# Performance work log

Measured on AMD Instinct MI355X. Metric: run time of the kernel, lower is better.

## Reference

```python
import jax, jax.numpy as jnp
import numpy as np

B = 1048576
H = 256


def _parity_W():
    # W[i,j,k] = 1 if (i+j+k+1) % 2 == 0  <=>  (i+j+k) odd
    idx = jnp.arange(2)
    s = idx[:, None, None] + idx[None, :, None] + idx[None, None, :]
    return (s % 2 == 1).astype(jnp.float32)


def setup_inputs() -> dict:
    key = jax.random.key(0)
    ks = jax.random.split(key, 7)
    x = jax.random.normal(ks[0], (B, 3), dtype=jnp.float32)
    w1 = jax.random.normal(ks[1], (H, 3), dtype=jnp.float32) * (1.0 / np.sqrt(3))
    b1 = jax.random.normal(ks[2], (H,), dtype=jnp.float32) * 0.01
    w2 = jax.random.normal(ks[3], (H, H), dtype=jnp.float32) * (1.0 / np.sqrt(H))
    b2 = jax.random.normal(ks[4], (H,), dtype=jnp.float32) * 0.01
    w3 = jax.random.normal(ks[5], (3, H), dtype=jnp.float32) * (1.0 / np.sqrt(H))
    b3 = jax.random.normal(ks[6], (3,), dtype=jnp.float32) * 0.01
    return {"x": x, "w1": w1, "b1": b1, "w2": w2, "b2": b2, "w3": w3, "b3": b3}


def reference(x, w1, b1, w2, b2, w3, b3):
    # MLP: 3 -> H -> H -> 3 with ReLU
    h = jax.nn.relu(x @ w1.T + b1)          # (B, H)
    h = jax.nn.relu(h @ w2.T + b2)          # (B, H)
    logitC = h @ w3.T + b3                  # (B, 3)

    eps = 1e-05
    sig = jax.nn.sigmoid(logitC)            # (B, 3)
    p_pos = (sig + eps) / (1.0 + 2.0 * eps)
    p_neg = (1.0 - sig + eps) / (1.0 + 2.0 * eps)
    p = jnp.stack([p_neg, p_pos], axis=-1)  # (B, 3, 2): per-concept Bernoulli probs

    W = _parity_W()                          # (2, 2, 2) XOR-parity indicator
    pred1 = jnp.einsum('bi,bj,bk,ijk->b', p[:, 0], p[:, 1], p[:, 2], W)  # (B,)
    pred = jnp.stack([1.0 - pred1, pred1], axis=1)  # (B, 2)
    pred = (pred + 0.001) / (1.0 + 2.0 * 0.001)
    return pred, logitC
```

## Files before the change

### kernel.cpp

```cpp
#include <hip/hip_runtime.h>

typedef _Float16 f16;
typedef _Float16 f16x8 __attribute__((ext_vector_type(8)));
typedef float f32x16 __attribute__((ext_vector_type(16)));
typedef unsigned int u32;
typedef unsigned int u32x4 __attribute__((ext_vector_type(4)));

#define THREADS 512
#define MTILE   128
#define NBLK    256

#define H1_OFF   0
#define XS_OFF   131072
#define PART_OFF 134144
#define LDS_BYTES 158720

template <int I0>
static __device__ __forceinline__ u32x4 relu_pack8(const f32x16& h) {
  const float c0 = fmaxf(h[I0+0], 0.f), c1 = fmaxf(h[I0+1], 0.f);
  const float c2 = fmaxf(h[I0+2], 0.f), c3 = fmaxf(h[I0+3], 0.f);
  const float c4 = fmaxf(h[I0+4], 0.f), c5 = fmaxf(h[I0+5], 0.f);
  const float c6 = fmaxf(h[I0+6], 0.f), c7 = fmaxf(h[I0+7], 0.f);
  u32 P = __builtin_bit_cast(u32, __builtin_amdgcn_cvt_pkrtz(c0, c1));
  u32 Q = __builtin_bit_cast(u32, __builtin_amdgcn_cvt_pkrtz(c2, c3));
  u32 R = __builtin_bit_cast(u32, __builtin_amdgcn_cvt_pkrtz(c4, c5));
  u32 S = __builtin_bit_cast(u32, __builtin_amdgcn_cvt_pkrtz(c6, c7));
  asm("v_permlane32_swap_b32 %0, %1" : "+v"(P), "+v"(R));
  asm("v_permlane32_swap_b32 %0, %1" : "+v"(Q), "+v"(S));
  u32x4 w; w[0] = P; w[1] = Q; w[2] = R; w[3] = S;
  return w;
}

__global__ __launch_bounds__(THREADS, 1)
void fused_mlp_parity(const float* __restrict__ x,
                      const float* __restrict__ w1,
                      const float* __restrict__ b1,
                      const float* __restrict__ w2,
                      const float* __restrict__ b2,
                      const float* __restrict__ w3,
                      const float* __restrict__ b3,
                      float* __restrict__ out, int Bsz) {
  __shared__ __align__(128) unsigned char lds[LDS_BYTES];
  const int tid  = threadIdx.x;
  const int lane = tid & 63;
  const int wave = tid >> 6;
  const int arow = lane & 31;
  const int half = lane >> 5;
  const int grp  = wave >> 2;

  const int ntiles = Bsz / MTILE;
  const int tpb    = ntiles / NBLK;
  const int t0     = blockIdx.x * tpb;

  float* xsf   = (float*)(lds + XS_OFF);
  float* partf = (float*)(lds + PART_OFF);

  {
    const float4* xg = (const float4*)x;
    if (tid < 96)                      ((float4*)xsf)[tid]            = xg[(size_t)t0*96 + tid];
    else if (tid >= 128 && tid < 224)  ((float4*)xsf)[96 + tid - 128] = xg[(size_t)(t0+1)*96 + (tid-128)];
  }

  const int col = (wave << 5) + arow;
  f16x8 w2A[16];
#pragma unroll
  for (int ks = 0; ks < 16; ++ks) {
    const float* src = w2 + (size_t)col*256 + ks*16 + half*8;
    float4 u0 = *(const float4*)src;
    float4 u1 = *(const float4*)(src + 4);
    f16x8 v;
    v[0]=(f16)u0.x; v[1]=(f16)u0.y; v[2]=(f16)u0.z; v[3]=(f16)u0.w;
    v[4]=(f16)u1.x; v[5]=(f16)u1.y; v[6]=(f16)u1.z; v[7]=(f16)u1.w;
    w2A[ks] = v;
  }
  f16x8 w1A = {};
  if (half == 0) {
    w1A[0] = (f16)w1[col*3+0]; w1A[1] = (f16)w1[col*3+1];
    w1A[2] = (f16)w1[col*3+2]; w1A[3] = (f16)b1[col];
  }
  f16x8 b2A = {};  if (half == 0) b2A[0] = (f16)b2[col];
  f16x8 ones = {}; if (half == 0) ones[0] = (f16)1.0f;
  f16x8 w3A[2];
#pragma unroll
  for (int q = 0; q < 2; ++q) {
    f16x8 v = {};
    if (arow < 3) {
#pragma unroll
      for (int j = 0; j < 8; ++j)
        v[j] = (f16)w3[arow*256 + (wave<<5) + q*16 + half*8 + j];
    }
    w3A[q] = v;
  }
  const float b3r0 = b3[0], b3r1 = b3[1], b3r2 = b3[2];
  const size_t outL = (size_t)Bsz * 2;
  const u32 rk = ((u32)(arow & 15)) << 4;
  const u32 cb = (u32)half << 4;

  auto PHASE_B = [&](int buf) {
    unsigned char* h1b = lds + H1_OFF + (u32)buf*65536;
    const float* xb_src = xsf + (u32)buf*384;
#pragma unroll
    for (int nt = 0; nt < 4; ++nt) {
      const int r = nt*32 + arow;
      f16x8 xb = {};
      if (half == 0) {
        const float* xr = xb_src + r*3;
        xb[0] = (f16)xr[0]; xb[1] = (f16)xr[1]; xb[2] = (f16)xr[2];
        xb[3] = (f16)1.0f;
      }
      f32x16 h = {};
      h = __builtin_amdgcn_mfma_f32_32x32x16_f16(w1A, xb, h, 0,0,0);
      const u32 rowbase = ((u32)r << 9);
      {
        u32x4 w = relu_pack8<0>(h);
        const u32 slot = (u32)(((wave<<5) + 0)*2 + half*16);
        *(u32x4*)(h1b + rowbase + (slot ^ rk)) = w;
      }
      {
        u32x4 w = relu_pack8<8>(h);
        const u32 slot = (u32)(((wave<<5) + 16)*2 + half*16);
        *(u32x4*)(h1b + rowbase + (slot ^ rk)) = w;
      }
    }
  };

  auto PHASE_CE = [&](int buf) {
    const unsigned char* h1b = lds + H1_OFF + (u32)buf*65536;
#pragma unroll
    for (int ntp = 0; ntp < 2; ++ntp) {
      f32x16 acc0, acc1;
      {
        f32x16 z = {};
        acc0 = __builtin_amdgcn_mfma_f32_32x32x16_f16(b2A, ones, z, 0,0,0);
        acc1 = __builtin_amdgcn_mfma_f32_32x32x16_f16(b2A, ones, z, 0,0,0);
      }
      const u32 row0 = (u32)((ntp*2 + 0)*32 + arow) << 9;
      const u32 row1 = (u32)((ntp*2 + 1)*32 + arow) << 9;
#pragma unroll
      for (int ks = 0; ks < 16; ++ks) {
        const u32 coff = ((((u32)ks) << 5) + cb) ^ rk;
        f16x8 fr0 = *(const f16x8*)(h1b + row0 + coff);
        f16x8 fr1 = *(const f16x8*)(h1b + row1 + coff);
        acc0 = __builtin_amdgcn_mfma_f32_32x32x16_f16(w2A[ks], fr0, acc0, 0,0,0);
        acc1 = __builtin_amdgcn_mfma_f32_32x32x16_f16(w2A[ks], fr1, acc1, 0,0,0);
      }
#pragma unroll
      for (int p = 0; p < 2; ++p) {
        const f32x16& a = p ? acc1 : acc0;
        const int nt = ntp*2 + p;
        f32x16 a3 = {};
        {
          u32x4 w = relu_pack8<0>(a);
          a3 = __builtin_amdgcn_mfma_f32_32x32x16_f16(w3A[0], __builtin_bit_cast(f16x8, w), a3, 0,0,0);
        }
        {
          u32x4 w = relu_pack8<8>(a);
          a3 = __builtin_amdgcn_mfma_f32_32x32x16_f16(w3A[1], __builtin_bit_cast(f16x8, w), a3, 0,0,0);
        }
        if (half == 0) {
          float* pr = partf + (u32)buf*3072 + (u32)((wave<<7) + nt*32 + arow)*3;
          pr[0] = a3[0]; pr[1] = a3[1]; pr[2] = a3[2];
        }
      }
    }
  };

  auto FINAL = [&](int pbuf, int tidx) {
    const int idx = tid - 256;
    if (idx >= 0 && idx < MTILE) {
      const int r = idx;
      const float* pb = partf + (u32)pbuf*3072;
      float l0 = b3r0, l1 = b3r1, l2 = b3r2;
#pragma unroll
      for (int w8 = 0; w8 < 8; ++w8) {
        const float* pr = pb + (u32)((w8<<7) + r)*3;
        l0 += pr[0]; l1 += pr[1]; l2 += pr[2];
      }
      const float inv1p2e = 1.0f / (1.0f + 2.0f * 1e-5f);
      const float tt0 = (1.0f - 2.0f / (1.0f + __expf(-l0))) * inv1p2e;
      const float tt1 = (1.0f - 2.0f / (1.0f + __expf(-l1))) * inv1p2e;
      const float tt2 = (1.0f - 2.0f / (1.0f + __expf(-l2))) * inv1p2e;
      const float pred1 = 0.5f * (1.0f - tt0 * tt1 * tt2);
      const size_t grow = (size_t)(t0 + tidx)*MTILE + r;
      float2 ov;
      ov.x = (1.0f - pred1 + 0.001f) * (1.0f / 1.002f);
      ov.y = (pred1 + 0.001f) * (1.0f / 1.002f);
      *(float2*)(out + grow*2) = ov;
      out[outL + grow*3 + 0] = l0;
      out[outL + grow*3 + 1] = l1;
      out[outL + grow*3 + 2] = l2;
    }
  };

  __syncthreads();
  PHASE_B(0);
  __syncthreads();

  for (int tl = 0; tl < tpb; ++tl) {
    const int cur = tl & 1, nxt = cur ^ 1;

    if (grp == 0) {
      PHASE_CE(cur);
      if (tl + 1 < tpb) PHASE_B(nxt);
      if (tl + 2 < tpb && tid >= 128 && tid < 224) {
        const int i = tid - 128;
        ((float4*)(xsf + (u32)cur*384))[i] =
            ((const float4*)x)[(size_t)(t0 + tl + 2)*96 + i];
      }
    } else {
      if (tl + 1 < tpb) PHASE_B(nxt);
      PHASE_CE(cur);
      if (tl > 0) FINAL(nxt, tl - 1);
    }
    __syncthreads();
  }

  FINAL((tpb - 1) & 1, tpb - 1);
}

extern "C" void kernel_launch(void* const* d_in, const int* in_sizes, int n_in,
                              void* d_out, int out_size, void* d_ws, size_t ws_size,
                              hipStream_t stream) {
  const float* x  = (const float*)d_in[0];
  const float* w1 = (const float*)d_in[1];
  const float* b1 = (const float*)d_in[2];
  const float* w2 = (const float*)d_in[3];
  const float* b2 = (const float*)d_in[4];
  const float* w3 = (const float*)d_in[5];
  const float* b3 = (const float*)d_in[6];
  float* out = (float*)d_out;
  const int Bsz = in_sizes[0] / 3;

  dim3 grid(NBLK), block(THREADS);
  fused_mlp_parity<<<grid, block, 0, stream>>>(x, w1, b1, w2, b2, w3, b3, out, Bsz);
}
```

Measured before the change: 218.9 us.

## Fold bias into accumulator init, packed f16 ReLU, spread FINAL across all waves

Several changes land together. ReLU now runs as packed f16 max after conversion, and the permlane swaps are dropped by reordering the w2/w3 K-layout loads to match. The two bias-init MFMAs per tile are replaced by a precomputed bias accumulator fed into the first K-step. The two wave groups no longer run in skewed order, so all waves run the same schedule with setprio around the MFMA loop. The FINAL epilogue is spread over all 512 threads, four lanes per row, with shuffles replacing the single-group serial reduction. The aim is to cut VALU/MFMA overhead and epilogue imbalance, at the cost of losing the intra-block phase staggering.

```diff
diff --git a/kernel.cpp b/kernel.cpp
--- a/kernel.cpp
+++ b/kernel.cpp
@@ -17,16 +17,14 @@
 
 template <int I0>
 static __device__ __forceinline__ u32x4 relu_pack8(const f32x16& h) {
-  const float c0 = fmaxf(h[I0+0], 0.f), c1 = fmaxf(h[I0+1], 0.f);
-  const float c2 = fmaxf(h[I0+2], 0.f), c3 = fmaxf(h[I0+3], 0.f);
-  const float c4 = fmaxf(h[I0+4], 0.f), c5 = fmaxf(h[I0+5], 0.f);
-  const float c6 = fmaxf(h[I0+6], 0.f), c7 = fmaxf(h[I0+7], 0.f);
-  u32 P = __builtin_bit_cast(u32, __builtin_amdgcn_cvt_pkrtz(c0, c1));
-  u32 Q = __builtin_bit_cast(u32, __builtin_amdgcn_cvt_pkrtz(c2, c3));
-  u32 R = __builtin_bit_cast(u32, __builtin_amdgcn_cvt_pkrtz(c4, c5));
-  u32 S = __builtin_bit_cast(u32, __builtin_amdgcn_cvt_pkrtz(c6, c7));
-  asm("v_permlane32_swap_b32 %0, %1" : "+v"(P), "+v"(R));
-  asm("v_permlane32_swap_b32 %0, %1" : "+v"(Q), "+v"(S));
+  u32 P = __builtin_bit_cast(u32, __builtin_amdgcn_cvt_pkrtz(h[I0+0], h[I0+1]));
+  u32 Q = __builtin_bit_cast(u32, __builtin_amdgcn_cvt_pkrtz(h[I0+2], h[I0+3]));
+  u32 R = __builtin_bit_cast(u32, __builtin_amdgcn_cvt_pkrtz(h[I0+4], h[I0+5]));
+  u32 S = __builtin_bit_cast(u32, __builtin_amdgcn_cvt_pkrtz(h[I0+6], h[I0+7]));
+  asm("v_pk_max_f16 %0, %0, 0" : "+v"(P));
+  asm("v_pk_max_f16 %0, %0, 0" : "+v"(Q));
+  asm("v_pk_max_f16 %0, %0, 0" : "+v"(R));
+  asm("v_pk_max_f16 %0, %0, 0" : "+v"(S));
   u32x4 w; w[0] = P; w[1] = Q; w[2] = R; w[3] = S;
   return w;
 }
@@ -46,7 +44,6 @@
   const int wave = tid >> 6;
   const int arow = lane & 31;
   const int half = lane >> 5;
-  const int grp  = wave >> 2;
 
   const int ntiles = Bsz / MTILE;
   const int tpb    = ntiles / NBLK;
@@ -61,13 +58,14 @@
     else if (tid >= 128 && tid < 224)  ((float4*)xsf)[96 + tid - 128] = xg[(size_t)(t0+1)*96 + (tid-128)];
   }
 
-  const int col = (wave << 5) + arow;
+  const int colbase = wave << 5;
+  const int col = colbase + arow;
   f16x8 w2A[16];
 #pragma unroll
   for (int ks = 0; ks < 16; ++ks) {
-    const float* src = w2 + (size_t)col*256 + ks*16 + half*8;
+    const float* src = w2 + (size_t)col*256 + ks*16 + half*4;
     float4 u0 = *(const float4*)src;
-    float4 u1 = *(const float4*)(src + 4);
+    float4 u1 = *(const float4*)(src + 8);
     f16x8 v;
     v[0]=(f16)u0.x; v[1]=(f16)u0.y; v[2]=(f16)u0.z; v[3]=(f16)u0.w;
     v[4]=(f16)u1.x; v[5]=(f16)u1.y; v[6]=(f16)u1.z; v[7]=(f16)u1.w;
@@ -78,8 +76,12 @@
     w1A[0] = (f16)w1[col*3+0]; w1A[1] = (f16)w1[col*3+1];
     w1A[2] = (f16)w1[col*3+2]; w1A[3] = (f16)b1[col];
   }
-  f16x8 b2A = {};  if (half == 0) b2A[0] = (f16)b2[col];
-  f16x8 ones = {}; if (half == 0) ones[0] = (f16)1.0f;
+  f32x16 biasInit;
+#pragma unroll
+  for (int reg = 0; reg < 16; ++reg) {
+    const int rowin32 = (reg & 3) + 8*(reg >> 2) + 4*half;
+    biasInit[reg] = (float)(f16)b2[colbase + rowin32];
+  }
   f16x8 w3A[2];
 #pragma unroll
   for (int q = 0; q < 2; ++q) {
@@ -87,7 +89,7 @@
     if (arow < 3) {
 #pragma unroll
       for (int j = 0; j < 8; ++j)
-        v[j] = (f16)w3[arow*256 + (wave<<5) + q*16 + half*8 + j];
+        v[j] = (f16)w3[arow*256 + colbase + q*16 + 4*half + (j&3) + 8*(j>>2)];
     }
     w3A[q] = v;
   }
@@ -113,12 +115,12 @@
       const u32 rowbase = ((u32)r << 9);
       {
         u32x4 w = relu_pack8<0>(h);
-        const u32 slot = (u32)(((wave<<5) + 0)*2 + half*16);
+        const u32 slot = (u32)((colbase + 0)*2 + half*16);
         *(u32x4*)(h1b + rowbase + (slot ^ rk)) = w;
       }
       {
         u32x4 w = relu_pack8<8>(h);
-        const u32 slot = (u32)(((wave<<5) + 16)*2 + half*16);
+        const u32 slot = (u32)((colbase + 16)*2 + half*16);
         *(u32x4*)(h1b + rowbase + (slot ^ rk)) = w;
       }
     }
@@ -128,22 +130,26 @@
     const unsigned char* h1b = lds + H1_OFF + (u32)buf*65536;
 #pragma unroll
     for (int ntp = 0; ntp < 2; ++ntp) {
-      f32x16 acc0, acc1;
-      {
-        f32x16 z = {};
-        acc0 = __builtin_amdgcn_mfma_f32_32x32x16_f16(b2A, ones, z, 0,0,0);
-        acc1 = __builtin_amdgcn_mfma_f32_32x32x16_f16(b2A, ones, z, 0,0,0);
-      }
       const u32 row0 = (u32)((ntp*2 + 0)*32 + arow) << 9;
       const u32 row1 = (u32)((ntp*2 + 1)*32 + arow) << 9;
-#pragma unroll
-      for (int ks = 0; ks < 16; ++ks) {
+      f32x16 acc0, acc1;
+      __builtin_amdgcn_s_setprio(1);
+      {
+        const u32 coff = cb ^ rk;
+        f16x8 fr0 = *(const f16x8*)(h1b + row0 + coff);
+        f16x8 fr1 = *(const f16x8*)(h1b + row1 + coff);
+        acc0 = __builtin_amdgcn_mfma_f32_32x32x16_f16(w2A[0], fr0, biasInit, 0,0,0);
+        acc1 = __builtin_amdgcn_mfma_f32_32x32x16_f16(w2A[0], fr1, biasInit, 0,0,0);
+      }
+#pragma unroll
+      for (int ks = 1; ks < 16; ++ks) {
         const u32 coff = ((((u32)ks) << 5) + cb) ^ rk;
         f16x8 fr0 = *(const f16x8*)(h1b + row0 + coff);
         f16x8 fr1 = *(const f16x8*)(h1b + row1 + coff);
         acc0 = __builtin_amdgcn_mfma_f32_32x32x16_f16(w2A[ks], fr0, acc0, 0,0,0);
         acc1 = __builtin_amdgcn_mfma_f32_32x32x16_f16(w2A[ks], fr1, acc1, 0,0,0);
       }
+      __builtin_amdgcn_s_setprio(0);
 #pragma unroll
       for (int p = 0; p < 2; ++p) {
         const f32x16& a = p ? acc1 : acc0;
@@ -166,29 +172,28 @@
   };
 
   auto FINAL = [&](int pbuf, int tidx) {
-    const int idx = tid - 256;
-    if (idx >= 0 && idx < MTILE) {
-      const int r = idx;
-      const float* pb = partf + (u32)pbuf*3072;
-      float l0 = b3r0, l1 = b3r1, l2 = b3r2;
-#pragma unroll
-      for (int w8 = 0; w8 < 8; ++w8) {
-        const float* pr = pb + (u32)((w8<<7) + r)*3;
-        l0 += pr[0]; l1 += pr[1]; l2 += pr[2];
-      }
+    const int row = tid >> 2, q = tid & 3;
+    const int qc = (q < 3) ? q : 2;
+    const float* pb = partf + (u32)pbuf*3072;
+    float l = (q == 0) ? b3r0 : ((q == 1) ? b3r1 : b3r2);
+#pragma unroll
+    for (int w8 = 0; w8 < 8; ++w8)
+      l += pb[(u32)((w8 << 7) + row)*3 + qc];
+    const size_t grow = (size_t)(t0 + tidx)*MTILE + row;
+    if (q < 3) out[outL + grow*3 + q] = l;
+    const int lbase = lane & 60;
+    const float l1v = __shfl(l, lbase + 1);
+    const float l2v = __shfl(l, lbase + 2);
+    if (q == 0) {
       const float inv1p2e = 1.0f / (1.0f + 2.0f * 1e-5f);
-      const float tt0 = (1.0f - 2.0f / (1.0f + __expf(-l0))) * inv1p2e;
-      const float tt1 = (1.0f - 2.0f / (1.0f + __expf(-l1))) * inv1p2e;
-      const float tt2 = (1.0f - 2.0f / (1.0f + __expf(-l2))) * inv1p2e;
+      const float tt0 = (1.0f - 2.0f / (1.0f + __expf(-l)))   * inv1p2e;
+      const float tt1 = (1.0f - 2.0f / (1.0f + __expf(-l1v))) * inv1p2e;
+      const float tt2 = (1.0f - 2.0f / (1.0f + __expf(-l2v))) * inv1p2e;
       const float pred1 = 0.5f * (1.0f - tt0 * tt1 * tt2);
-      const size_t grow = (size_t)(t0 + tidx)*MTILE + r;
       float2 ov;
       ov.x = (1.0f - pred1 + 0.001f) * (1.0f / 1.002f);
       ov.y = (pred1 + 0.001f) * (1.0f / 1.002f);
       *(float2*)(out + grow*2) = ov;
-      out[outL + grow*3 + 0] = l0;
-      out[outL + grow*3 + 1] = l1;
-      out[outL + grow*3 + 2] = l2;
     }
   };
 
@@ -199,19 +204,14 @@
   for (int tl = 0; tl < tpb; ++tl) {
     const int cur = tl & 1, nxt = cur ^ 1;
 
-    if (grp == 0) {
-      PHASE_CE(cur);
-      if (tl + 1 < tpb) PHASE_B(nxt);
-      if (tl + 2 < tpb && tid >= 128 && tid < 224) {
-        const int i = tid - 128;
-        ((float4*)(xsf + (u32)cur*384))[i] =
-            ((const float4*)x)[(size_t)(t0 + tl + 2)*96 + i];
-      }
-    } else {
-      if (tl + 1 < tpb) PHASE_B(nxt);
-      PHASE_CE(cur);
-      if (tl > 0) FINAL(nxt, tl - 1);
-    }
+    PHASE_CE(cur);
+    if (tl + 1 < tpb) PHASE_B(nxt);
+    if (tl + 2 < tpb && tid >= 416) {
+      const int i = tid - 416;
+      ((float4*)(xsf + (u32)cur*384))[i] =
+          ((const float4*)x)[(size_t)(t0 + tl + 2)*96 + i];
+    }
+    if (tl > 0) FINAL(nxt, tl - 1);
     __syncthreads();
   }
 
```

Result: slower. 239.6 us (+9.5%).
